# Optimization experiments

Hardware: AMD Instinct MI355X
Metric: run time of the kernel (lower is better)

## Reference

```python
import jax, jax.numpy as jnp
import numpy as np

RNN = 64

def linear(x, W, b):
    return x @ W.T + b

def sample_logprob(key, logits):
    # Categorical(softmax(logits)): sample + log_prob of the sample
    s = jax.random.categorical(key, logits)
    lp = jnp.take_along_axis(jax.nn.log_softmax(logits, -1), s[:, None], 1)[:, 0]
    return s, lp

def lstm_encode(inst, embed, W_ih, W_hh, b_ih, b_hh):
    # torch.nn.LSTMCell unrolled over the sequence; gate order i,f,g,o
    x = embed[inst]                              # [B,S,64]
    B = inst.shape[0]
    def step(carry, xt):
        h, c = carry
        gates = xt @ W_ih.T + b_ih + h @ W_hh.T + b_hh   # [B,256]
        i, f, g, o = jnp.split(gates, 4, axis=-1)
        c = jax.nn.sigmoid(f) * c + jax.nn.sigmoid(i) * jnp.tanh(g)
        h = jax.nn.sigmoid(o) * jnp.tanh(c)
        return (h, c), None
    h0 = jnp.zeros((B, RNN), x.dtype)
    (h, _), _ = jax.lax.scan(step, (h0, h0), jnp.swapaxes(x, 0, 1))
    return h

def setup_inputs():
    key = jax.random.key(0)
    ks = jax.random.split(key, 20)
    B, S, V = 16384, 32, 1000
    def nrm(k, shape, scale=0.05):
        return jax.random.normal(k, shape, jnp.float32) * scale
    return {
        "inst0": jax.random.randint(ks[0], (B, S), 0, V + 1),
        "inst1": jax.random.randint(ks[1], (B, S), 0, V + 1),
        "canvas0": jax.random.randint(ks[2], (B, 25, 4), 0, 5).astype(jnp.int32),
        "canvas1": jax.random.randint(ks[3], (B, 25, 4), 0, 5).astype(jnp.int32),
        "ref": jax.random.randint(ks[4], (B, 4), 0, 5).astype(jnp.int32),
        "embed": nrm(ks[5], (V + 1, RNN)),
        "W_ih": nrm(ks[6], (4 * RNN, RNN)), "W_hh": nrm(ks[7], (4 * RNN, RNN)),
        "b_ih": jnp.zeros(4 * RNN), "b_hh": jnp.zeros(4 * RNN),
        "Wc": nrm(ks[8], (3, RNN)), "bc": jnp.zeros(3),
        "Ws": nrm(ks[9], (3, RNN)), "bs": jnp.zeros(3),
        "Wl": nrm(ks[10], (25, RNN)), "bl": jnp.zeros(25),
        "Wr1": nrm(ks[11], (32, RNN + 4)), "br1": jnp.zeros(32),
        "Wr2": nrm(ks[12], (1, 32)), "br2": jnp.zeros(1),
        "Wp": nrm(ks[13], (8, RNN)), "bp": jnp.zeros(8),
    }

def reference(inst0, inst1, canvas0, canvas1, ref, embed, W_ih, W_hh, b_ih, b_hh,
              Wc, bc, Ws, bs, Wl, bl, Wr1, br1, Wr2, br2, Wp, bp):
    B = inst0.shape[0]
    kk = jax.random.split(jax.random.key(42), 7)
    final_canvas = canvas1                                   # [B,25,4]

    def step_rewards(loc_predict, color_sample, shape_sample):
        valid = (loc_predict >= 0) & (loc_predict < 25)
        pt = jnp.take_along_axis(final_canvas,
                                 jnp.clip(loc_predict, 0, 24)[:, None, None],
                                 axis=1)[:, 0]               # [B,4]
        ok = valid & (pt.sum(-1) >= 0)
        loc_r = jnp.where(ok, 1.0, -1.0)
        col_r = jnp.where(ok, jnp.where(color_sample == pt[:, 0], 1.0, -1.0), 0.0)
        shp_r = jnp.where(ok, jnp.where(shape_sample == pt[:, 1], 1.0, -1.0), 0.0)
        return loc_r, col_r, shp_r

    # ---- dialog step 0: absolute location ----
    h0 = lstm_encode(inst0, embed, W_ih, W_hh, b_ih, b_hh)
    cs0, clp0 = sample_logprob(kk[0], linear(h0, Wc, bc))
    ss0, slp0 = sample_logprob(kk[1], linear(h0, Ws, bs))
    loc0, llp0 = sample_logprob(kk[2], linear(h0, Wl, bl))
    loc_r0, col_r0, _ = step_rewards(loc0, cs0, ss0)

    # ---- dialog step 1: relative location w.r.t. attended ref object ----
    h1 = lstm_encode(inst1, embed, W_ih, W_hh, b_ih, b_hh)
    cs1, clp1 = sample_logprob(kk[3], linear(h1, Wc, bc))
    ss1, slp1 = sample_logprob(kk[4], linear(h1, Ws, bs))
    ls1, llp1 = sample_logprob(kk[5], linear(h1, Wp, bp))    # 8-way offset
    prev = canvas0.astype(h1.dtype)                          # [B,25,4]
    feat = jnp.concatenate([jnp.broadcast_to(h1[:, None, :], (B, 25, RNN)), prev], 2)  # [B,25,68]
    att_logits = (jax.nn.relu(feat @ Wr1.T + br1) @ Wr2.T + br2)[:, :, 0]              # [B,25]
    att_sample, alp1 = sample_logprob(kk[6], att_logits)
    ref_obj = jnp.take_along_axis(canvas0, att_sample[:, None, None], axis=1)[:, 0]    # [B,4]
    att_reward = ((ref_obj == ref).sum(-1) == 4).astype(jnp.float32) * 2.0 - 1.0
    offsets = jnp.array([[-1, 0], [1, 0], [0, 1], [0, -1],
                         [-1, -1], [-1, 1], [1, -1], [1, 1]], jnp.int32)
    off = offsets[ls1]
    loc1 = (ref_obj[:, 2] + off[:, 0]) * 5 + (ref_obj[:, 3] + off[:, 1])
    loc_r1, col_r1, _ = step_rewards(loc1, cs1, ss1)

    logp = jnp.stack([clp0, slp0, llp0, clp1, slp1, llp1, alp1])          # [7,B]
    # NB: original appends step_loc_reward into shape_rewards (kept verbatim)
    rew = jnp.stack([loc_r0, col_r0, loc_r0, loc_r1, col_r1, loc_r1, att_reward])  # [7,B]
    return logp, rew
```

## Files before the change

kernel.cpp:

```cpp
#include <hip/hip_runtime.h>
#include <hip/hip_bf16.h>
#include <stdint.h>
#include <math.h>

#define NB 16384
#define NSEQ 32
#define NV 1001
#define NROWS 32768

#define CHK 272
#define RTG (8 * CHK)
#define SPL (2 * RTG)
#define HBUF (3 * SPL)

typedef __attribute__((ext_vector_type(8))) short bf16x8;
typedef __attribute__((ext_vector_type(4))) float f32x4;

__device__ __forceinline__ void tf2x32(uint32_t k0, uint32_t k1,
                                       uint32_t x0, uint32_t x1,
                                       uint32_t& o0, uint32_t& o1) {
  const uint32_t ks0 = k0, ks1 = k1, ks2 = k0 ^ k1 ^ 0x1BD11BDAu;
  x0 += ks0; x1 += ks1;
  const int rA[4] = {13, 15, 26, 6};
  const int rB[4] = {17, 29, 16, 24};
#pragma unroll
  for (int i = 0; i < 4; ++i) { x0 += x1; x1 = (x1 << rA[i]) | (x1 >> (32 - rA[i])); x1 ^= x0; }
  x0 += ks1; x1 += ks2 + 1u;
#pragma unroll
  for (int i = 0; i < 4; ++i) { x0 += x1; x1 = (x1 << rB[i]) | (x1 >> (32 - rB[i])); x1 ^= x0; }
  x0 += ks2; x1 += ks0 + 2u;
#pragma unroll
  for (int i = 0; i < 4; ++i) { x0 += x1; x1 = (x1 << rA[i]) | (x1 >> (32 - rA[i])); x1 ^= x0; }
  x0 += ks0; x1 += ks1 + 3u;
#pragma unroll
  for (int i = 0; i < 4; ++i) { x0 += x1; x1 = (x1 << rB[i]) | (x1 >> (32 - rB[i])); x1 ^= x0; }
  x0 += ks1; x1 += ks2 + 4u;
#pragma unroll
  for (int i = 0; i < 4; ++i) { x0 += x1; x1 = (x1 << rA[i]) | (x1 >> (32 - rA[i])); x1 ^= x0; }
  o0 = x0 + ks2; o1 = x1 + ks0 + 5u;
}

__device__ __forceinline__ float gumbel_from_bits(uint32_t bits) {
  uint32_t fb = (bits >> 9) | 0x3f800000u;
  float u = __uint_as_float(fb) - 1.0f;
  u = fmaxf(u, 1.17549435e-38f);
  return -logf(-logf(u));
}

__device__ __forceinline__ float sigm(float x) { return 1.0f / (1.0f + __expf(-x)); }
__device__ __forceinline__ float tanh_(float x) {
  float e = __expf(2.0f * x);
  return 1.0f - 2.0f / (e + 1.0f);
}

__device__ __forceinline__ float dot64(const float* __restrict__ w, const float* h) {
  float a = 0.f;
#pragma unroll
  for (int k = 0; k < 64; ++k) a = fmaf(w[k], h[k], a);
  return a;
}

__device__ __forceinline__ unsigned short bfbits(float x, float& xf) {
  __hip_bfloat16 hb = __float2bfloat16(x);
  xf = __bfloat162float(hb);
  unsigned short u;
  __builtin_memcpy(&u, &hb, 2);
  return u;
}

template <int N>
__device__ __forceinline__ void samp_team(const float* lg, int g, int C,
                                          uint32_t k0, uint32_t k1, int b,
                                          int& sOut, float& lpOut) {
  float m = -__builtin_inff();
#pragma unroll
  for (int i = 0; i < N; ++i) m = fmaxf(m, lg[i]);
  m = fmaxf(m, __shfl_xor(m, 1));
  m = fmaxf(m, __shfl_xor(m, 2));
  float se = 0.f;
#pragma unroll
  for (int i = 0; i < N; ++i) se += expf(lg[i] - m);
  se += __shfl_xor(se, 1);
  se += __shfl_xor(se, 2);
  const float lse = logf(se);
  float bz = -__builtin_inff(), bl = 0.f;
  int bi = 0x7fffffff;
#pragma unroll
  for (int i = 0; i < N; ++i) {
    const int c = g + 4 * i;
    uint32_t o0, o1; tf2x32(k0, k1, 0u, (uint32_t)(b * C + c), o0, o1);
    const float z = lg[i] + gumbel_from_bits(o0 ^ o1);
    if (z > bz || (z == bz && c < bi)) { bz = z; bi = c; bl = lg[i]; }
  }
#pragma unroll
  for (int d = 1; d <= 2; d <<= 1) {
    const float z2 = __shfl_xor(bz, d);
    const int i2 = __shfl_xor(bi, d);
    const float l2 = __shfl_xor(bl, d);
    if (z2 > bz || (z2 == bz && i2 < bi)) { bz = z2; bi = i2; bl = l2; }
  }
  sOut = bi;
  lpOut = (bl - m) - lse;
}

__global__ __launch_bounds__(256) void k_prep(
    const float* __restrict__ embed, const float* __restrict__ W_ih,
    const float* __restrict__ W_hh, const float* __restrict__ b_ih,
    const float* __restrict__ b_hh, float* __restrict__ embedWi,
    unsigned short* __restrict__ Wsp) {
  if (blockIdx.x >= NV) {
    int idx = (blockIdx.x - NV) * 256 + threadIdx.x;
    int s = idx >> 14;
    int rem = idx & 16383;
    int jp = rem >> 6, m = rem & 63;
    int kc = m >> 5, q = (m >> 3) & 3, p = m & 7;
    int k = kc * 32 + q * 8 + ((p >> 1) + ((p & 1) << 2));
    int j = (jp & 3) * 64 + (jp >> 2);
    float w = W_hh[j * 64 + k];
    float f1, f2, f3;
    unsigned short b1 = bfbits(w, f1);
    unsigned short b2 = bfbits(w - f1, f2);
    unsigned short b3 = bfbits(w - f1 - f2, f3);
    Wsp[idx] = (s == 0) ? b1 : (s == 1) ? b2 : b3;
    return;
  }
  __shared__ float er[64];
  int v = blockIdx.x;
  if (threadIdx.x < 64) er[threadIdx.x] = embed[v * 64 + threadIdx.x];
  __syncthreads();
  int jp = threadIdx.x;
  int j = (jp & 3) * 64 + (jp >> 2);
  float a = b_ih[j] + b_hh[j];
#pragma unroll
  for (int k = 0; k < 64; ++k) a = fmaf(W_ih[j * 64 + k], er[k], a);
  embedWi[v * 256 + jp] = a;
}

__global__ __launch_bounds__(512, 4) void k_lstm(
    const int* __restrict__ inst0, const int* __restrict__ inst1,
    const float* __restrict__ embedWi, const unsigned short* __restrict__ Wsp,
    float* __restrict__ hT) {
  extern __shared__ char smc[];
  int* idsb = (int*)(smc + 2 * HBUF);

  const int tid = threadIdx.x;
  const int lane = tid & 63;
  const int e8 = tid >> 6;
  const int n15 = lane & 15;
  const int quad = lane >> 4;
  const int blk = blockIdx.x;
  const int rowbase = blk * 32;
  const int rb = (blk & 511) * 32;
  const int* __restrict__ inst = (blk < 512) ? inst0 : inst1;

  bf16x8 afr[2][2][3];
#pragma unroll
  for (int jt = 0; jt < 2; ++jt) {
    const int jrow = (e8 * 2 + jt) * 16 + n15;
#pragma unroll
    for (int kc = 0; kc < 2; ++kc)
#pragma unroll
      for (int s = 0; s < 3; ++s)
        afr[jt][kc][s] =
            *(const bf16x8*)(Wsp + ((s * 256 + jrow) * 64 + kc * 32 + quad * 8));
  }

  for (int i = tid; i < HBUF / 4; i += 512) ((float*)smc)[i] = 0.f;
  if (tid < 32) idsb[tid] = inst[(rb + tid) * NSEQ];

  float cst[4];
#pragma unroll
  for (int i = 0; i < 4; ++i) cst[i] = 0.f;

  __syncthreads();

#pragma unroll 1
  for (int t = 0; t < NSEQ; ++t) {
    const char* __restrict__ hbr = smc + (t & 1) * HBUF;
    char* __restrict__ hbw = smc + ((t & 1) ^ 1) * HBUF;
    const bool last = (t == NSEQ - 1);

    if (tid < 32 && t + 1 < NSEQ)
      idsb[((t + 1) & 1) * 32 + tid] = inst[(rb + tid) * NSEQ + t + 1];

    float4 esc[2], esn[2];
    {
      const int v0 = idsb[(t & 1) * 32 + n15];
#pragma unroll
      for (int jt = 0; jt < 2; ++jt)
        esc[jt] = *(const float4*)(embedWi + v0 * 256 +
                                   (e8 * 8 + jt * 4 + quad) * 4);
    }

#pragma unroll
    for (int rt = 0; rt < 2; ++rt) {
      if (rt < 1) {
        const int vn = idsb[(t & 1) * 32 + 16 + n15];
#pragma unroll
        for (int jt = 0; jt < 2; ++jt)
          esn[jt] = *(const float4*)(embedWi + vn * 256 +
                                     (e8 * 8 + jt * 4 + quad) * 4);
      }
      bf16x8 bfr[2][3];
#pragma unroll
      for (int kc = 0; kc < 2; ++kc)
#pragma unroll
        for (int s = 0; s < 3; ++s)
          bfr[kc][s] = *(const bf16x8*)(hbr + s * SPL + rt * RTG +
                                        (kc * 4 + quad) * CHK + n15 * 16);
      f32x4 C2[2];
#pragma unroll
      for (int jt = 0; jt < 2; ++jt) C2[jt] = (f32x4){0.f, 0.f, 0.f, 0.f};
#pragma unroll
      for (int jt = 0; jt < 2; ++jt) {
#pragma unroll
        for (int kc = 0; kc < 2; ++kc) {
          f32x4 acc = C2[jt];
          acc = __builtin_amdgcn_mfma_f32_16x16x32_bf16(afr[jt][kc][0], bfr[kc][2], acc, 0, 0, 0);
          acc = __builtin_amdgcn_mfma_f32_16x16x32_bf16(afr[jt][kc][2], bfr[kc][0], acc, 0, 0, 0);
          acc = __builtin_amdgcn_mfma_f32_16x16x32_bf16(afr[jt][kc][1], bfr[kc][1], acc, 0, 0, 0);
          acc = __builtin_amdgcn_mfma_f32_16x16x32_bf16(afr[jt][kc][0], bfr[kc][1], acc, 0, 0, 0);
          acc = __builtin_amdgcn_mfma_f32_16x16x32_bf16(afr[jt][kc][1], bfr[kc][0], acc, 0, 0, 0);
          acc = __builtin_amdgcn_mfma_f32_16x16x32_bf16(afr[jt][kc][0], bfr[kc][0], acc, 0, 0, 0);
          C2[jt] = acc;
        }
      }

      float hval[2];
      unsigned short s1[2], s2[2], s3[2];
#pragma unroll
      for (int jt = 0; jt < 2; ++jt) {
        const float gi = C2[jt].x + esc[jt].x;
        const float gf = C2[jt].y + esc[jt].y;
        const float gg = C2[jt].z + esc[jt].z;
        const float go = C2[jt].w + esc[jt].w;
        const float ci = sigm(gf) * cst[jt * 2 + rt] + sigm(gi) * tanh_(gg);
        cst[jt * 2 + rt] = ci;
        const float h = sigm(go) * tanh_(ci);
        hval[jt] = h;
        float f1, f2, f3;
        s1[jt] = bfbits(h, f1);
        s2[jt] = bfbits(h - f1, f2);
        s3[jt] = bfbits(h - f1 - f2, f3);
      }
      char* base = hbw + rt * RTG + e8 * CHK + n15 * 16 + quad * 4;
      *(uint32_t*)(base + 0 * SPL) = (uint32_t)s1[0] | ((uint32_t)s1[1] << 16);
      *(uint32_t*)(base + 1 * SPL) = (uint32_t)s2[0] | ((uint32_t)s2[1] << 16);
      *(uint32_t*)(base + 2 * SPL) = (uint32_t)s3[0] | ((uint32_t)s3[1] << 16);
      if (last) {
#pragma unroll
        for (int jt = 0; jt < 2; ++jt)
          hT[(e8 * 8 + jt * 4 + quad) * NROWS + rowbase + rt * 16 + n15] = hval[jt];
      }
      esc[0] = esn[0]; esc[1] = esn[1];
    }
    __syncthreads();
  }
}

__global__ __launch_bounds__(256) void k_heads(
    const int* __restrict__ canvas0, const int* __restrict__ canvas1,
    const int* __restrict__ ref,
    const float* __restrict__ Wc, const float* __restrict__ bc,
    const float* __restrict__ Ws, const float* __restrict__ bs,
    const float* __restrict__ Wl, const float* __restrict__ bl,
    const float* __restrict__ Wr1, const float* __restrict__ br1,
    const float* __restrict__ Wr2, const float* __restrict__ br2,
    const float* __restrict__ Wp, const float* __restrict__ bp,
    const float* __restrict__ hT, float* __restrict__ out) {
  const int tid = threadIdx.x;
  const int g = tid & 3;
  const int s = blockIdx.x & 1;
  const int b = (blockIdx.x >> 1) * 64 + (tid >> 2);
  const float NEG = -__builtin_inff();

  uint32_t kk0[7], kk1[7];
#pragma unroll
  for (int i = 0; i < 7; ++i) {
    uint32_t o0, o1; tf2x32(0u, 42u, 0u, (uint32_t)i, o0, o1);
    kk0[i] = o0; kk1[i] = o1;
  }

  float h[64];
#pragma unroll
  for (int u = 0; u < 64; ++u) h[u] = hT[u * NROWS + s * NB + b];

  float lgc[1], lgs[1];
  lgc[0] = (g < 3) ? (bc[g] + dot64(Wc + g * 64, h)) : NEG;
  lgs[0] = (g < 3) ? (bs[g] + dot64(Ws + g * 64, h)) : NEG;

  if (s == 0) {
    int cs0, ss0, loc0; float clp0, slp0, llp0;
    samp_team<1>(lgc, g, 3, kk0[0], kk1[0], b, cs0, clp0);
    samp_team<1>(lgs, g, 3, kk0[1], kk1[1], b, ss0, slp0);
    float lgl[7];
#pragma unroll
    for (int i = 0; i < 7; ++i) {
      const int cc = g + 4 * i;
      lgl[i] = (cc < 25) ? (bl[cc] + dot64(Wl + cc * 64, h)) : NEG;
    }
    samp_team<7>(lgl, g, 25, kk0[2], kk1[2], b, loc0, llp0);

    if (g == 0) {
      const int p0 = min(max(loc0, 0), 24);
      const int4 pt = ((const int4*)(canvas1 + b * 100))[p0];
      const bool ok0 = (loc0 >= 0) && (loc0 < 25) && (pt.x + pt.y + pt.z + pt.w >= 0);
      const float loc_r0 = ok0 ? 1.f : -1.f;
      const float col_r0 = ok0 ? ((cs0 == pt.x) ? 1.f : -1.f) : 0.f;
      out[0 * NB + b] = clp0;
      out[1 * NB + b] = slp0;
      out[2 * NB + b] = llp0;
      out[7 * NB + b] = loc_r0;
      out[8 * NB + b] = col_r0;
      out[9 * NB + b] = loc_r0;
    }
  } else {
    int cs1, ss1, ls1; float clp1, slp1, llp1;
    samp_team<1>(lgc, g, 3, kk0[3], kk1[3], b, cs1, clp1);
    samp_team<1>(lgs, g, 3, kk0[4], kk1[4], b, ss1, slp1);
    float lgp[2];
#pragma unroll
    for (int i = 0; i < 2; ++i) {
      const int cc = g + 4 * i;
      lgp[i] = bp[cc] + dot64(Wp + cc * 64, h);
    }
    samp_team<2>(lgp, g, 8, kk0[5], kk1[5], b, ls1, llp1);

    float uv8[8], w64[8], w65[8], w66[8], w67[8], wr2[8];
#pragma unroll
    for (int i = 0; i < 8; ++i) {
      const int j = g + 4 * i;
      uv8[i] = br1[j] + dot64(Wr1 + j * 68, h);
      const float* wr = Wr1 + j * 68 + 64;
      w64[i] = wr[0]; w65[i] = wr[1]; w66[i] = wr[2]; w67[i] = wr[3];
      wr2[i] = Wr2[j];
    }
    float lgA[7];
#pragma unroll
    for (int i = 0; i < 7; ++i) lgA[i] = NEG;
    const float b2 = br2[0];
#pragma unroll
    for (int p = 0; p < 25; ++p) {
      const int4 c4 = ((const int4*)(canvas0 + b * 100))[p];
      const float f0 = (float)c4.x, f1 = (float)c4.y;
      const float f2 = (float)c4.z, f3 = (float)c4.w;
      float part = 0.f;
#pragma unroll
      for (int i = 0; i < 8; ++i) {
        float hj = uv8[i];
        hj = fmaf(w64[i], f0, hj);
        hj = fmaf(w65[i], f1, hj);
        hj = fmaf(w66[i], f2, hj);
        hj = fmaf(w67[i], f3, hj);
        part = fmaf(wr2[i], fmaxf(hj, 0.f), part);
      }
      part += __shfl_xor(part, 1);
      part += __shfl_xor(part, 2);
      const float ap = b2 + part;
      if ((p & 3) == g) lgA[p >> 2] = ap;
    }
    int att_s; float alp1;
    samp_team<7>(lgA, g, 25, kk0[6], kk1[6], b, att_s, alp1);

    if (g == 0) {
      const int4 r4 = ((const int4*)(canvas0 + b * 100))[att_s];
      const int4 rr = *(const int4*)(ref + b * 4);
      const bool match = (r4.x == rr.x) && (r4.y == rr.y) &&
                         (r4.z == rr.z) && (r4.w == rr.w);
      const float att_reward = match ? 1.f : -1.f;
      const int ox = (int)((0x22001120u >> (ls1 * 4)) & 0xFu) - 1;
      const int oy = (int)((0x20200211u >> (ls1 * 4)) & 0xFu) - 1;
      const int loc1 = (r4.z + ox) * 5 + (r4.w + oy);
      const int p1 = min(max(loc1, 0), 24);
      const int4 q4 = ((const int4*)(canvas1 + b * 100))[p1];
      const bool ok1 = (loc1 >= 0) && (loc1 < 25) && (q4.x + q4.y + q4.z + q4.w >= 0);
      const float loc_r1 = ok1 ? 1.f : -1.f;
      const float col_r1 = ok1 ? ((cs1 == q4.x) ? 1.f : -1.f) : 0.f;
      out[3 * NB + b]  = clp1;
      out[4 * NB + b]  = slp1;
      out[5 * NB + b]  = llp1;
      out[6 * NB + b]  = alp1;
      out[10 * NB + b] = loc_r1;
      out[11 * NB + b] = col_r1;
      out[12 * NB + b] = loc_r1;
      out[13 * NB + b] = att_reward;
    }
  }
}

extern "C" void kernel_launch(void* const* d_in, const int* in_sizes, int n_in,
                              void* d_out, int out_size, void* d_ws, size_t ws_size,
                              hipStream_t stream) {
  const int* inst0 = (const int*)d_in[0];
  const int* inst1 = (const int*)d_in[1];
  const int* canvas0 = (const int*)d_in[2];
  const int* canvas1 = (const int*)d_in[3];
  const int* ref = (const int*)d_in[4];
  const float* embed = (const float*)d_in[5];
  const float* W_ih = (const float*)d_in[6];
  const float* W_hh = (const float*)d_in[7];
  const float* b_ih = (const float*)d_in[8];
  const float* b_hh = (const float*)d_in[9];
  const float* Wc = (const float*)d_in[10];
  const float* bc = (const float*)d_in[11];
  const float* Ws = (const float*)d_in[12];
  const float* bs = (const float*)d_in[13];
  const float* Wl = (const float*)d_in[14];
  const float* bl = (const float*)d_in[15];
  const float* Wr1 = (const float*)d_in[16];
  const float* br1 = (const float*)d_in[17];
  const float* Wr2 = (const float*)d_in[18];
  const float* br2 = (const float*)d_in[19];
  const float* Wp = (const float*)d_in[20];
  const float* bp = (const float*)d_in[21];

  float* ws = (float*)d_ws;
  float* embedWi = ws;
  unsigned short* Wsp = (unsigned short*)(ws + NV * 256);
  float* hT = ws + NV * 256 + 24576;
  float* out = (float*)d_out;

  const size_t ldsBytes = 2 * HBUF + 256;
  k_prep<<<NV + 192, 256, 0, stream>>>(embed, W_ih, W_hh, b_ih, b_hh, embedWi, Wsp);
  k_lstm<<<1024, 512, ldsBytes, stream>>>(inst0, inst1, embedWi, Wsp, hT);
  k_heads<<<512, 256, 0, stream>>>(canvas0, canvas1, ref, Wc, bc, Ws, bs,
                                   Wl, bl, Wr1, br1, Wr2, br2, Wp, bp, hT, out);
}
```

Before: 422.1 us.

## Interleave LSTM MFMA tiles with cell math and preload token ids to LDS

Restructures each LSTM timestep to issue the four 16x16 MFMA accumulations as separate tiles and to run the gate nonlinearities of finished tiles while later tiles' MFMAs are in flight. Explicit sched_group_barrier hints set the interleaving. All 32x32 token ids for the block are loaded into LDS once, transposed, instead of one global load per step. It also uses packed bf16x2 conversions for the three-way h split, and rebuilds the final hidden state from LDS after the loop instead of branching on the last step. This costs more LDS and a hand-pinned schedule, and the final h is now the sum of three bf16 parts rather than the exact fp32 value.

```diff
diff --git a/kernel.cpp b/kernel.cpp
--- a/kernel.cpp
+++ b/kernel.cpp
@@ -66,6 +66,24 @@
   unsigned short u;
   __builtin_memcpy(&u, &hb, 2);
   return u;
+}
+
+__device__ __forceinline__ uint32_t pkbf(float a, float b) {
+  __hip_bfloat162 p = __float22bfloat162_rn(make_float2(a, b));
+  uint32_t u; __builtin_memcpy(&u, &p, 4);
+  return u;
+}
+__device__ __forceinline__ float lo16f(uint32_t w) { return __uint_as_float(w << 16); }
+__device__ __forceinline__ float hi16f(uint32_t w) { return __uint_as_float(w & 0xffff0000u); }
+
+__device__ __forceinline__ float lcell(const f32x4 A, const float4 es, float& c) {
+  const float gi = A.x + es.x;
+  const float gf = A.y + es.y;
+  const float gg = A.z + es.z;
+  const float go = A.w + es.w;
+  const float ci = sigm(gf) * c + sigm(gi) * tanh_(gg);
+  c = ci;
+  return sigm(go) * tanh_(ci);
 }
 
 template <int N>
@@ -141,7 +159,7 @@
     const float* __restrict__ embedWi, const unsigned short* __restrict__ Wsp,
     float* __restrict__ hT) {
   extern __shared__ char smc[];
-  int* idsb = (int*)(smc + 2 * HBUF);
+  int* idst = (int*)(smc + 2 * HBUF);
 
   const int tid = threadIdx.x;
   const int lane = tid & 63;
@@ -166,7 +184,11 @@
   }
 
   for (int i = tid; i < HBUF / 4; i += 512) ((float*)smc)[i] = 0.f;
-  if (tid < 32) idsb[tid] = inst[(rb + tid) * NSEQ];
+
+  for (int i = tid; i < 1024; i += 512) {
+    const int row = i >> 5, tt = i & 31;
+    idst[tt * 32 + row] = inst[rb * NSEQ + i];
+  }
 
   float cst[4];
 #pragma unroll
@@ -178,83 +200,125 @@
   for (int t = 0; t < NSEQ; ++t) {
     const char* __restrict__ hbr = smc + (t & 1) * HBUF;
     char* __restrict__ hbw = smc + ((t & 1) ^ 1) * HBUF;
-    const bool last = (t == NSEQ - 1);
-
-    if (tid < 32 && t + 1 < NSEQ)
-      idsb[((t + 1) & 1) * 32 + tid] = inst[(rb + tid) * NSEQ + t + 1];
-
+
+    const int v0 = idst[t * 32 + n15];
+    const int vn = idst[t * 32 + 16 + n15];
     float4 esc[2], esn[2];
+#pragma unroll
+    for (int jt = 0; jt < 2; ++jt) {
+      esc[jt] = *(const float4*)(embedWi + v0 * 256 + (e8 * 8 + jt * 4 + quad) * 4);
+      esn[jt] = *(const float4*)(embedWi + vn * 256 + (e8 * 8 + jt * 4 + quad) * 4);
+    }
+
+    bf16x8 b0[2][3], b1[2][3];
+#pragma unroll
+    for (int kc = 0; kc < 2; ++kc)
+#pragma unroll
+      for (int s = 0; s < 3; ++s) {
+        b0[kc][s] = *(const bf16x8*)(hbr + s * SPL + 0 * RTG +
+                                     (kc * 4 + quad) * CHK + n15 * 16);
+        b1[kc][s] = *(const bf16x8*)(hbr + s * SPL + 1 * RTG +
+                                     (kc * 4 + quad) * CHK + n15 * 16);
+      }
+
+    f32x4 a00 = (f32x4){0.f, 0.f, 0.f, 0.f};
+#pragma unroll
+    for (int kc = 0; kc < 2; ++kc) {
+      a00 = __builtin_amdgcn_mfma_f32_16x16x32_bf16(afr[0][kc][0], b0[kc][2], a00, 0, 0, 0);
+      a00 = __builtin_amdgcn_mfma_f32_16x16x32_bf16(afr[0][kc][2], b0[kc][0], a00, 0, 0, 0);
+      a00 = __builtin_amdgcn_mfma_f32_16x16x32_bf16(afr[0][kc][1], b0[kc][1], a00, 0, 0, 0);
+      a00 = __builtin_amdgcn_mfma_f32_16x16x32_bf16(afr[0][kc][0], b0[kc][1], a00, 0, 0, 0);
+      a00 = __builtin_amdgcn_mfma_f32_16x16x32_bf16(afr[0][kc][1], b0[kc][0], a00, 0, 0, 0);
+      a00 = __builtin_amdgcn_mfma_f32_16x16x32_bf16(afr[0][kc][0], b0[kc][0], a00, 0, 0, 0);
+    }
+
+    f32x4 a01 = (f32x4){0.f, 0.f, 0.f, 0.f};
+#pragma unroll
+    for (int kc = 0; kc < 2; ++kc) {
+      a01 = __builtin_amdgcn_mfma_f32_16x16x32_bf16(afr[1][kc][0], b0[kc][2], a01, 0, 0, 0);
+      a01 = __builtin_amdgcn_mfma_f32_16x16x32_bf16(afr[1][kc][2], b0[kc][0], a01, 0, 0, 0);
+      a01 = __builtin_amdgcn_mfma_f32_16x16x32_bf16(afr[1][kc][1], b0[kc][1], a01, 0, 0, 0);
+      a01 = __builtin_amdgcn_mfma_f32_16x16x32_bf16(afr[1][kc][0], b0[kc][1], a01, 0, 0, 0);
+      a01 = __builtin_amdgcn_mfma_f32_16x16x32_bf16(afr[1][kc][1], b0[kc][0], a01, 0, 0, 0);
+      a01 = __builtin_amdgcn_mfma_f32_16x16x32_bf16(afr[1][kc][0], b0[kc][0], a01, 0, 0, 0);
+    }
+    const float hv00 = lcell(a00, esc[0], cst[0]);
+
+    f32x4 a10 = (f32x4){0.f, 0.f, 0.f, 0.f};
+#pragma unroll
+    for (int kc = 0; kc < 2; ++kc) {
+      a10 = __builtin_amdgcn_mfma_f32_16x16x32_bf16(afr[0][kc][0], b1[kc][2], a10, 0, 0, 0);
+      a10 = __builtin_amdgcn_mfma_f32_16x16x32_bf16(afr[0][kc][2], b1[kc][0], a10, 0, 0, 0);
+      a10 = __builtin_amdgcn_mfma_f32_16x16x32_bf16(afr[0][kc][1], b1[kc][1], a10, 0, 0, 0);
+      a10 = __builtin_amdgcn_mfma_f32_16x16x32_bf16(afr[0][kc][0], b1[kc][1], a10, 0, 0, 0);
+      a10 = __builtin_amdgcn_mfma_f32_16x16x32_bf16(afr[0][kc][1], b1[kc][0], a10, 0, 0, 0);
+      a10 = __builtin_amdgcn_mfma_f32_16x16x32_bf16(afr[0][kc][0], b1[kc][0], a10, 0, 0, 0);
+    }
+    const float hv10 = lcell(a01, esc[1], cst[2]);
     {
-      const int v0 = idsb[(t & 1) * 32 + n15];
-#pragma unroll
-      for (int jt = 0; jt < 2; ++jt)
-        esc[jt] = *(const float4*)(embedWi + v0 * 256 +
-                                   (e8 * 8 + jt * 4 + quad) * 4);
-    }
-
-#pragma unroll
-    for (int rt = 0; rt < 2; ++rt) {
-      if (rt < 1) {
-        const int vn = idsb[(t & 1) * 32 + 16 + n15];
-#pragma unroll
-        for (int jt = 0; jt < 2; ++jt)
-          esn[jt] = *(const float4*)(embedWi + vn * 256 +
-                                     (e8 * 8 + jt * 4 + quad) * 4);
-      }
-      bf16x8 bfr[2][3];
-#pragma unroll
-      for (int kc = 0; kc < 2; ++kc)
-#pragma unroll
-        for (int s = 0; s < 3; ++s)
-          bfr[kc][s] = *(const bf16x8*)(hbr + s * SPL + rt * RTG +
-                                        (kc * 4 + quad) * CHK + n15 * 16);
-      f32x4 C2[2];
-#pragma unroll
-      for (int jt = 0; jt < 2; ++jt) C2[jt] = (f32x4){0.f, 0.f, 0.f, 0.f};
-#pragma unroll
-      for (int jt = 0; jt < 2; ++jt) {
-#pragma unroll
-        for (int kc = 0; kc < 2; ++kc) {
-          f32x4 acc = C2[jt];
-          acc = __builtin_amdgcn_mfma_f32_16x16x32_bf16(afr[jt][kc][0], bfr[kc][2], acc, 0, 0, 0);
-          acc = __builtin_amdgcn_mfma_f32_16x16x32_bf16(afr[jt][kc][2], bfr[kc][0], acc, 0, 0, 0);
-          acc = __builtin_amdgcn_mfma_f32_16x16x32_bf16(afr[jt][kc][1], bfr[kc][1], acc, 0, 0, 0);
-          acc = __builtin_amdgcn_mfma_f32_16x16x32_bf16(afr[jt][kc][0], bfr[kc][1], acc, 0, 0, 0);
-          acc = __builtin_amdgcn_mfma_f32_16x16x32_bf16(afr[jt][kc][1], bfr[kc][0], acc, 0, 0, 0);
-          acc = __builtin_amdgcn_mfma_f32_16x16x32_bf16(afr[jt][kc][0], bfr[kc][0], acc, 0, 0, 0);
-          C2[jt] = acc;
-        }
-      }
-
-      float hval[2];
-      unsigned short s1[2], s2[2], s3[2];
-#pragma unroll
-      for (int jt = 0; jt < 2; ++jt) {
-        const float gi = C2[jt].x + esc[jt].x;
-        const float gf = C2[jt].y + esc[jt].y;
-        const float gg = C2[jt].z + esc[jt].z;
-        const float go = C2[jt].w + esc[jt].w;
-        const float ci = sigm(gf) * cst[jt * 2 + rt] + sigm(gi) * tanh_(gg);
-        cst[jt * 2 + rt] = ci;
-        const float h = sigm(go) * tanh_(ci);
-        hval[jt] = h;
-        float f1, f2, f3;
-        s1[jt] = bfbits(h, f1);
-        s2[jt] = bfbits(h - f1, f2);
-        s3[jt] = bfbits(h - f1 - f2, f3);
-      }
-      char* base = hbw + rt * RTG + e8 * CHK + n15 * 16 + quad * 4;
-      *(uint32_t*)(base + 0 * SPL) = (uint32_t)s1[0] | ((uint32_t)s1[1] << 16);
-      *(uint32_t*)(base + 1 * SPL) = (uint32_t)s2[0] | ((uint32_t)s2[1] << 16);
-      *(uint32_t*)(base + 2 * SPL) = (uint32_t)s3[0] | ((uint32_t)s3[1] << 16);
-      if (last) {
-#pragma unroll
-        for (int jt = 0; jt < 2; ++jt)
-          hT[(e8 * 8 + jt * 4 + quad) * NROWS + rowbase + rt * 16 + n15] = hval[jt];
-      }
-      esc[0] = esn[0]; esc[1] = esn[1];
-    }
+      const uint32_t w1 = pkbf(hv00, hv10);
+      float d0 = hv00 - lo16f(w1), d1 = hv10 - hi16f(w1);
+      const uint32_t w2 = pkbf(d0, d1);
+      d0 -= lo16f(w2); d1 -= hi16f(w2);
+      const uint32_t w3 = pkbf(d0, d1);
+      char* base = hbw + 0 * RTG + e8 * CHK + n15 * 16 + quad * 4;
+      *(uint32_t*)(base + 0 * SPL) = w1;
+      *(uint32_t*)(base + 1 * SPL) = w2;
+      *(uint32_t*)(base + 2 * SPL) = w3;
+    }
+
+    f32x4 a11 = (f32x4){0.f, 0.f, 0.f, 0.f};
+#pragma unroll
+    for (int kc = 0; kc < 2; ++kc) {
+      a11 = __builtin_amdgcn_mfma_f32_16x16x32_bf16(afr[1][kc][0], b1[kc][2], a11, 0, 0, 0);
+      a11 = __builtin_amdgcn_mfma_f32_16x16x32_bf16(afr[1][kc][2], b1[kc][0], a11, 0, 0, 0);
+      a11 = __builtin_amdgcn_mfma_f32_16x16x32_bf16(afr[1][kc][1], b1[kc][1], a11, 0, 0, 0);
+      a11 = __builtin_amdgcn_mfma_f32_16x16x32_bf16(afr[1][kc][0], b1[kc][1], a11, 0, 0, 0);
+      a11 = __builtin_amdgcn_mfma_f32_16x16x32_bf16(afr[1][kc][1], b1[kc][0], a11, 0, 0, 0);
+      a11 = __builtin_amdgcn_mfma_f32_16x16x32_bf16(afr[1][kc][0], b1[kc][0], a11, 0, 0, 0);
+    }
+    const float hv01 = lcell(a10, esn[0], cst[1]);
+
+    const float hv11 = lcell(a11, esn[1], cst[3]);
+    {
+      const uint32_t w1 = pkbf(hv01, hv11);
+      float d0 = hv01 - lo16f(w1), d1 = hv11 - hi16f(w1);
+      const uint32_t w2 = pkbf(d0, d1);
+      d0 -= lo16f(w2); d1 -= hi16f(w2);
+      const uint32_t w3 = pkbf(d0, d1);
+      char* base = hbw + 1 * RTG + e8 * CHK + n15 * 16 + quad * 4;
+      *(uint32_t*)(base + 0 * SPL) = w1;
+      *(uint32_t*)(base + 1 * SPL) = w2;
+      *(uint32_t*)(base + 2 * SPL) = w3;
+    }
+
+    __builtin_amdgcn_sched_group_barrier(0x100, 14, 0);
+    __builtin_amdgcn_sched_group_barrier(0x020, 4, 0);
+#pragma unroll
+    for (int i = 0; i < 12; ++i) {
+      __builtin_amdgcn_sched_group_barrier(0x008, 1, 0);
+      __builtin_amdgcn_sched_group_barrier(0x100, 1, 0);
+    }
+#pragma unroll
+    for (int i = 0; i < 36; ++i) {
+      __builtin_amdgcn_sched_group_barrier(0x008, 1, 0);
+      __builtin_amdgcn_sched_group_barrier(0x002, 4, 0);
+    }
+    __builtin_amdgcn_sched_group_barrier(0x200, 6, 0);
+
     __syncthreads();
+  }
+
+#pragma unroll
+  for (int rt = 0; rt < 2; ++rt) {
+    const char* base = smc + rt * RTG + e8 * CHK + n15 * 16 + quad * 4;
+    const uint32_t w1 = *(const uint32_t*)(base + 0 * SPL);
+    const uint32_t w2 = *(const uint32_t*)(base + 1 * SPL);
+    const uint32_t w3 = *(const uint32_t*)(base + 2 * SPL);
+    const float hv0 = lo16f(w1) + lo16f(w2) + lo16f(w3);
+    const float hv1 = hi16f(w1) + hi16f(w2) + hi16f(w3);
+    hT[(e8 * 8 + 0 * 4 + quad) * NROWS + rowbase + rt * 16 + n15] = hv0;
+    hT[(e8 * 8 + 1 * 4 + quad) * NROWS + rowbase + rt * 16 + n15] = hv1;
   }
 }
 
@@ -420,7 +484,7 @@
   float* hT = ws + NV * 256 + 24576;
   float* out = (float*)d_out;
 
-  const size_t ldsBytes = 2 * HBUF + 256;
+  const size_t ldsBytes = 2 * HBUF + 4096;
   k_prep<<<NV + 192, 256, 0, stream>>>(embed, W_ih, W_hh, b_ih, b_hh, embedWi, Wsp);
   k_lstm<<<1024, 512, ldsBytes, stream>>>(inst0, inst1, embedWi, Wsp, hT);
   k_heads<<<512, 256, 0, stream>>>(canvas0, canvas1, ref, Wc, bc, Ws, bs,
```

New measurement: 423.3 us. No clear change (+0.3%).

## Restructure LSTM kernel to one wave per 16 rows with register-resident hidden state

Applied to the files above, without the earlier changes.

The LSTM recurrence now runs one 64-lane wave per 16 batch rows. Each wave computes all 256 gates itself, keeps the hidden state in registers and redistributes it between steps with cross-lane shuffles. This removes the LDS double buffer and the block-wide barrier that the old 512-thread block needed every time step. In exchange, weight fragments are reloaded from global memory/cache on each step instead of staying resident in registers, and each wave does more serial MFMA work with fewer waves per row group.

```diff
diff --git a/kernel.cpp b/kernel.cpp
--- a/kernel.cpp
+++ b/kernel.cpp
@@ -7,11 +7,6 @@
 #define NSEQ 32
 #define NV 1001
 #define NROWS 32768
-
-#define CHK 272
-#define RTG (8 * CHK)
-#define SPL (2 * RTG)
-#define HBUF (3 * SPL)
 
 typedef __attribute__((ext_vector_type(8))) short bf16x8;
 typedef __attribute__((ext_vector_type(4))) float f32x4;
@@ -66,6 +61,16 @@
   unsigned short u;
   __builtin_memcpy(&u, &hb, 2);
   return u;
+}
+
+__device__ __forceinline__ float lcell(const f32x4 A, const float4 es, float& c) {
+  const float gi = A.x + es.x;
+  const float gf = A.y + es.y;
+  const float gg = A.z + es.z;
+  const float go = A.w + es.w;
+  const float ci = sigm(gf) * c + sigm(gi) * tanh_(gg);
+  c = ci;
+  return sigm(go) * tanh_(ci);
 }
 
 template <int N>
@@ -136,125 +141,126 @@
   embedWi[v * 256 + jp] = a;
 }
 
-__global__ __launch_bounds__(512, 4) void k_lstm(
+#define MFMA16(A_, B_, C_) __builtin_amdgcn_mfma_f32_16x16x32_bf16(A_, B_, C_, 0, 0, 0)
+__global__ __launch_bounds__(64, 2) void k_lstm(
     const int* __restrict__ inst0, const int* __restrict__ inst1,
     const float* __restrict__ embedWi, const unsigned short* __restrict__ Wsp,
     float* __restrict__ hT) {
-  extern __shared__ char smc[];
-  int* idsb = (int*)(smc + 2 * HBUF);
-
-  const int tid = threadIdx.x;
-  const int lane = tid & 63;
-  const int e8 = tid >> 6;
-  const int n15 = lane & 15;
-  const int quad = lane >> 4;
-  const int blk = blockIdx.x;
-  const int rowbase = blk * 32;
-  const int rb = (blk & 511) * 32;
-  const int* __restrict__ inst = (blk < 512) ? inst0 : inst1;
-
-  bf16x8 afr[2][2][3];
-#pragma unroll
-  for (int jt = 0; jt < 2; ++jt) {
-    const int jrow = (e8 * 2 + jt) * 16 + n15;
-#pragma unroll
-    for (int kc = 0; kc < 2; ++kc)
-#pragma unroll
-      for (int s = 0; s < 3; ++s)
-        afr[jt][kc][s] =
-            *(const bf16x8*)(Wsp + ((s * 256 + jrow) * 64 + kc * 32 + quad * 8));
-  }
-
-  for (int i = tid; i < HBUF / 4; i += 512) ((float*)smc)[i] = 0.f;
-  if (tid < 32) idsb[tid] = inst[(rb + tid) * NSEQ];
-
-  float cst[4];
-#pragma unroll
-  for (int i = 0; i < 4; ++i) cst[i] = 0.f;
-
-  __syncthreads();
+  const int lane = threadIdx.x & 63;
+  const int q = lane >> 4;
+  const int n = lane & 15;
+  const int grow = blockIdx.x * 16 + n;
+  const int* __restrict__ inst = (blockIdx.x < 1024) ? inst0 : inst1;
+  const int rb_row = grow & (NB - 1);
+
+  float cst[16];
+#pragma unroll
+  for (int i = 0; i < 16; ++i) cst[i] = 0.f;
+
+  uint32_t bw[2][3][4];
+#pragma unroll
+  for (int kc = 0; kc < 2; ++kc)
+#pragma unroll
+    for (int s = 0; s < 3; ++s)
+#pragma unroll
+      for (int w = 0; w < 4; ++w) bw[kc][s][w] = 0u;
+
+  int vcur = inst[rb_row * NSEQ];
 
 #pragma unroll 1
   for (int t = 0; t < NSEQ; ++t) {
-    const char* __restrict__ hbr = smc + (t & 1) * HBUF;
-    char* __restrict__ hbw = smc + ((t & 1) ^ 1) * HBUF;
     const bool last = (t == NSEQ - 1);
-
-    if (tid < 32 && t + 1 < NSEQ)
-      idsb[((t + 1) & 1) * 32 + tid] = inst[(rb + tid) * NSEQ + t + 1];
-
-    float4 esc[2], esn[2];
-    {
-      const int v0 = idsb[(t & 1) * 32 + n15];
-#pragma unroll
-      for (int jt = 0; jt < 2; ++jt)
-        esc[jt] = *(const float4*)(embedWi + v0 * 256 +
-                                   (e8 * 8 + jt * 4 + quad) * 4);
-    }
-
-#pragma unroll
-    for (int rt = 0; rt < 2; ++rt) {
-      if (rt < 1) {
-        const int vn = idsb[(t & 1) * 32 + 16 + n15];
-#pragma unroll
-        for (int jt = 0; jt < 2; ++jt)
-          esn[jt] = *(const float4*)(embedWi + vn * 256 +
-                                     (e8 * 8 + jt * 4 + quad) * 4);
+    const int vnxt = inst[rb_row * NSEQ + ((t + 1) & 31)];
+
+    bf16x8 B[2][3];
+#pragma unroll
+    for (int kc = 0; kc < 2; ++kc)
+#pragma unroll
+      for (int s = 0; s < 3; ++s) {
+        union { uint32_t u[4]; bf16x8 v; } tmp;
+#pragma unroll
+        for (int w = 0; w < 4; ++w) tmp.u[w] = bw[kc][s][w];
+        B[kc][s] = tmp.v;
       }
-      bf16x8 bfr[2][3];
-#pragma unroll
-      for (int kc = 0; kc < 2; ++kc)
-#pragma unroll
-        for (int s = 0; s < 3; ++s)
-          bfr[kc][s] = *(const bf16x8*)(hbr + s * SPL + rt * RTG +
-                                        (kc * 4 + quad) * CHK + n15 * 16);
-      f32x4 C2[2];
-#pragma unroll
-      for (int jt = 0; jt < 2; ++jt) C2[jt] = (f32x4){0.f, 0.f, 0.f, 0.f};
-#pragma unroll
-      for (int jt = 0; jt < 2; ++jt) {
-#pragma unroll
-        for (int kc = 0; kc < 2; ++kc) {
-          f32x4 acc = C2[jt];
-          acc = __builtin_amdgcn_mfma_f32_16x16x32_bf16(afr[jt][kc][0], bfr[kc][2], acc, 0, 0, 0);
-          acc = __builtin_amdgcn_mfma_f32_16x16x32_bf16(afr[jt][kc][2], bfr[kc][0], acc, 0, 0, 0);
-          acc = __builtin_amdgcn_mfma_f32_16x16x32_bf16(afr[jt][kc][1], bfr[kc][1], acc, 0, 0, 0);
-          acc = __builtin_amdgcn_mfma_f32_16x16x32_bf16(afr[jt][kc][0], bfr[kc][1], acc, 0, 0, 0);
-          acc = __builtin_amdgcn_mfma_f32_16x16x32_bf16(afr[jt][kc][1], bfr[kc][0], acc, 0, 0, 0);
-          acc = __builtin_amdgcn_mfma_f32_16x16x32_bf16(afr[jt][kc][0], bfr[kc][0], acc, 0, 0, 0);
-          C2[jt] = acc;
+
+    uint32_t Wown[2][4][3];
+    unsigned short pb1 = 0, pb2 = 0, pb3 = 0;
+
+#pragma unroll
+    for (int jt = 0; jt < 16; ++jt) {
+      const unsigned short* wp = Wsp + (jt * 16 + n) * 64 + q * 8;
+      const bf16x8 A00 = *(const bf16x8*)(wp);
+      const bf16x8 A01 = *(const bf16x8*)(wp + 32);
+      const bf16x8 A10 = *(const bf16x8*)(wp + 16384);
+      const bf16x8 A11 = *(const bf16x8*)(wp + 16384 + 32);
+      const bf16x8 A20 = *(const bf16x8*)(wp + 32768);
+      const bf16x8 A21 = *(const bf16x8*)(wp + 32768 + 32);
+      const float4 es = *(const float4*)(embedWi + vcur * 256 + jt * 16 + q * 4);
+
+      f32x4 acc = (f32x4){0.f, 0.f, 0.f, 0.f};
+      acc = MFMA16(A00, B[0][2], acc);
+      acc = MFMA16(A20, B[0][0], acc);
+      acc = MFMA16(A10, B[0][1], acc);
+      acc = MFMA16(A00, B[0][1], acc);
+      acc = MFMA16(A10, B[0][0], acc);
+      acc = MFMA16(A00, B[0][0], acc);
+      acc = MFMA16(A01, B[1][2], acc);
+      acc = MFMA16(A21, B[1][0], acc);
+      acc = MFMA16(A11, B[1][1], acc);
+      acc = MFMA16(A01, B[1][1], acc);
+      acc = MFMA16(A11, B[1][0], acc);
+      acc = MFMA16(A01, B[1][0], acc);
+
+      const float hv = lcell(acc, es, cst[jt]);
+
+      if (last) {
+        hT[(4 * jt + q) * NROWS + grow] = hv;
+      } else {
+        float f1, f2, f3x;
+        const unsigned short b1 = bfbits(hv, f1);
+        const unsigned short b2 = bfbits(hv - f1, f2);
+        const unsigned short b3 = bfbits(hv - f1 - f2, f3x);
+        if (jt & 1) {
+          constexpr int dummy = 0; (void)dummy;
+          const int p_ = jt >> 1;
+          const int kc_ = p_ >> 2, qd_ = p_ & 3;
+          Wown[kc_][qd_][0] = (uint32_t)pb1 | ((uint32_t)b1 << 16);
+          Wown[kc_][qd_][1] = (uint32_t)pb2 | ((uint32_t)b2 << 16);
+          Wown[kc_][qd_][2] = (uint32_t)pb3 | ((uint32_t)b3 << 16);
+        } else {
+          pb1 = b1; pb2 = b2; pb3 = b3;
         }
       }
-
-      float hval[2];
-      unsigned short s1[2], s2[2], s3[2];
-#pragma unroll
-      for (int jt = 0; jt < 2; ++jt) {
-        const float gi = C2[jt].x + esc[jt].x;
-        const float gf = C2[jt].y + esc[jt].y;
-        const float gg = C2[jt].z + esc[jt].z;
-        const float go = C2[jt].w + esc[jt].w;
-        const float ci = sigm(gf) * cst[jt * 2 + rt] + sigm(gi) * tanh_(gg);
-        cst[jt * 2 + rt] = ci;
-        const float h = sigm(go) * tanh_(ci);
-        hval[jt] = h;
-        float f1, f2, f3;
-        s1[jt] = bfbits(h, f1);
-        s2[jt] = bfbits(h - f1, f2);
-        s3[jt] = bfbits(h - f1 - f2, f3);
-      }
-      char* base = hbw + rt * RTG + e8 * CHK + n15 * 16 + quad * 4;
-      *(uint32_t*)(base + 0 * SPL) = (uint32_t)s1[0] | ((uint32_t)s1[1] << 16);
-      *(uint32_t*)(base + 1 * SPL) = (uint32_t)s2[0] | ((uint32_t)s2[1] << 16);
-      *(uint32_t*)(base + 2 * SPL) = (uint32_t)s3[0] | ((uint32_t)s3[1] << 16);
-      if (last) {
-#pragma unroll
-        for (int jt = 0; jt < 2; ++jt)
-          hT[(e8 * 8 + jt * 4 + quad) * NROWS + rowbase + rt * 16 + n15] = hval[jt];
-      }
-      esc[0] = esn[0]; esc[1] = esn[1];
-    }
-    __syncthreads();
+    }
+    vcur = vnxt;
+
+    if (!last) {
+#pragma unroll
+      for (int kc = 0; kc < 2; ++kc)
+#pragma unroll
+        for (int s = 0; s < 3; ++s) {
+          const uint32_t a0 = Wown[kc][0][s], a1 = Wown[kc][1][s];
+          const uint32_t a2 = Wown[kc][2][s], a3 = Wown[kc][3][s];
+          const uint32_t t0 = (uint32_t)__shfl_xor((int)a2, 32);
+          const uint32_t t1 = (uint32_t)__shfl_xor((int)a3, 32);
+          const uint32_t t2 = (uint32_t)__shfl_xor((int)a0, 32);
+          const uint32_t t3 = (uint32_t)__shfl_xor((int)a1, 32);
+          const bool hiq = (q & 2) != 0;
+          const uint32_t c0 = hiq ? t0 : a0;
+          const uint32_t c1 = hiq ? t1 : a1;
+          const uint32_t c2 = hiq ? a2 : t2;
+          const uint32_t c3 = hiq ? a3 : t3;
+          const uint32_t u0 = (uint32_t)__shfl_xor((int)c1, 16);
+          const uint32_t u1 = (uint32_t)__shfl_xor((int)c0, 16);
+          const uint32_t u2 = (uint32_t)__shfl_xor((int)c3, 16);
+          const uint32_t u3 = (uint32_t)__shfl_xor((int)c2, 16);
+          const bool oq = (q & 1) != 0;
+          bw[kc][s][0] = oq ? u0 : c0;
+          bw[kc][s][1] = oq ? c1 : u1;
+          bw[kc][s][2] = oq ? u2 : c2;
+          bw[kc][s][3] = oq ? c3 : u3;
+        }
+    }
   }
 }
 
@@ -420,9 +426,8 @@
   float* hT = ws + NV * 256 + 24576;
   float* out = (float*)d_out;
 
-  const size_t ldsBytes = 2 * HBUF + 256;
   k_prep<<<NV + 192, 256, 0, stream>>>(embed, W_ih, W_hh, b_ih, b_hh, embedWi, Wsp);
-  k_lstm<<<1024, 512, ldsBytes, stream>>>(inst0, inst1, embedWi, Wsp, hT);
+  k_lstm<<<2048, 64, 0, stream>>>(inst0, inst1, embedWi, Wsp, hT);
   k_heads<<<512, 256, 0, stream>>>(canvas0, canvas1, ref, Wc, bc, Ws, bs,
                                    Wl, bl, Wr1, br1, Wr2, br2, Wp, bp, hT, out);
 }
```

New measurement: 965.3 us. +128.7%, slower.
